# Performance work log

Hardware: AMD Instinct MI355X
Metric: run time of the kernel (lower is better)

The kernel has to match this reference:

```python
import jax, jax.numpy as jnp
import numpy as np

EMBED_DIM = 1024
NUM_HEADS = 16
HEAD_DIM = EMBED_DIM // NUM_HEADS


def setup_inputs() -> dict:
    key = jax.random.key(0)
    k1, k2, k3, k4, k5 = jax.random.split(key, 5)
    B, T, C = 4, 2048, EMBED_DIM
    scale = 1.0 / np.sqrt(C)
    return {
        "x": jax.random.normal(k1, (B, T, C), dtype=jnp.float32),
        "W_qkv": jax.random.normal(k2, (3 * C, C), dtype=jnp.float32) * scale,
        "b_qkv": jax.random.normal(k3, (3 * C,), dtype=jnp.float32) * 0.02,
        "W_proj": jax.random.normal(k4, (C, C), dtype=jnp.float32) * scale,
        "b_proj": jax.random.normal(k5, (C,), dtype=jnp.float32) * 0.02,
    }


def reference(x, W_qkv, b_qkv, W_proj, b_proj):
    B, T, C = x.shape
    H, D = NUM_HEADS, HEAD_DIM
    qkv = x @ W_qkv.T + b_qkv                      # [B,T,3C]
    q, k, v = jnp.split(qkv, 3, axis=-1)
    q = q.reshape(B, T, H, D).transpose(0, 2, 1, 3)  # [B,H,T,D]
    k = k.reshape(B, T, H, D).transpose(0, 2, 1, 3)
    v = v.reshape(B, T, H, D).transpose(0, 2, 1, 3)
    scores = jnp.einsum("bhqd,bhkd->bhqk", q, k) / np.sqrt(D)  # [B,H,T,T]
    causal = jnp.tril(jnp.ones((T, T), dtype=bool))
    scores = jnp.where(causal, scores, -jnp.inf)
    attn = jax.nn.softmax(scores, axis=-1)
    out = jnp.einsum("bhqk,bhkd->bhqd", attn, v)   # [B,H,T,D]
    out = out.transpose(0, 2, 1, 3).reshape(B, T, C)
    return out @ W_proj.T + b_proj
```

## Files before the change

kernel.cpp:

```cpp
#include <hip/hip_runtime.h>
#include <math.h>

#define EMBED 1024
#define NHEAD 16
#define HDIM  64
#define SEQT  2048
#define BATCH 4

typedef __bf16 bf16x4 __attribute__((ext_vector_type(4)));
typedef __bf16 bf16x8 __attribute__((ext_vector_type(8)));
typedef float  f32x4  __attribute__((ext_vector_type(4)));

#define AS1 __attribute__((address_space(1)))
#define AS3 __attribute__((address_space(3)))
#define GLD_LDS16(gp, lp) __builtin_amdgcn_global_load_lds( \
    (const AS1 unsigned int*)(gp), (AS3 unsigned int*)(lp), 16, 0, 0)

#define QSCALE 0.180336880f

__device__ __forceinline__ unsigned short f2bf_hw(float f) {
    union { __bf16 h; unsigned short u; } c; c.h = (__bf16)f; return c.u;
}

__global__ __launch_bounds__(256)
void cvt_all(const float* __restrict__ x, const float* __restrict__ wq,
             const float* __restrict__ wp,
             unsigned short* __restrict__ xb, unsigned short* __restrict__ wqb,
             unsigned short* __restrict__ wpb)
{
    const int N1 = 2097152;
    const int N2 = 786432;
    int i = blockIdx.x * 256 + threadIdx.x;
    const float4* src; ushort4* dst; int j;
    if (i < N1)            { src = (const float4*)x;  dst = (ushort4*)xb;  j = i; }
    else if (i < N1 + N2)  { src = (const float4*)wq; dst = (ushort4*)wqb; j = i - N1; }
    else                   { src = (const float4*)wp; dst = (ushort4*)wpb; j = i - N1 - N2; }
    float4 v = src[j];
    ushort4 o;
    o.x = f2bf_hw(v.x); o.y = f2bf_hw(v.y); o.z = f2bf_hw(v.z); o.w = f2bf_hw(v.w);
    dst[j] = o;
}

template<int MODE>
__global__ __launch_bounds__(256)
void gemm_bt_mfma(const unsigned short* __restrict__ A, const unsigned short* __restrict__ Bw,
                  const float* __restrict__ bias,
                  void* out0, void* out1, void* out2,
                  int M, int N, int K)
{
    __shared__ __align__(16) unsigned short Asm[2][128 * 32];
    __shared__ __align__(16) unsigned short Bsm[2][128 * 32];

    const int tid  = threadIdx.x;
    const int lane = tid & 63;
    const int wave = tid >> 6;
    const int wm = wave >> 1, wn = wave & 1;
    const int col = lane & 15, quad = lane >> 4;
    const long m0 = (long)blockIdx.y * 128, n0 = (long)blockIdx.x * 128;

    f32x4 acc[4][4];
#pragma unroll
    for (int mi = 0; mi < 4; mi++)
#pragma unroll
        for (int ni = 0; ni < 4; ni++) acc[mi][ni] = (f32x4){0.f, 0.f, 0.f, 0.f};

    const int lrow = tid >> 2;
    const int lcol = ((tid & 3) ^ ((tid >> 3) & 3)) * 8;
    const unsigned short* Ag = A + (m0 + lrow) * K + lcol;
    const unsigned short* Bg = Bw + (n0 + lrow) * K + lcol;

    const int rsw = (quad ^ ((col >> 1) & 3)) * 8;

    GLD_LDS16(Ag,                &Asm[0][0] + tid * 8);
    GLD_LDS16(Ag + (long)64 * K, &Asm[0][0] + 2048 + tid * 8);
    GLD_LDS16(Bg,                &Bsm[0][0] + tid * 8);
    GLD_LDS16(Bg + (long)64 * K, &Bsm[0][0] + 2048 + tid * 8);

    const int iters = K >> 5;
    for (int it = 0; it < iters; it++) {
        const int cur = it & 1;
        __builtin_amdgcn_s_waitcnt(0x0F70);
        __syncthreads();
        if (it + 1 < iters) {
            const int kk = (it + 1) * 32, nxt = cur ^ 1;
            GLD_LDS16(Ag + kk,                &Asm[nxt][0] + tid * 8);
            GLD_LDS16(Ag + (long)64 * K + kk, &Asm[nxt][0] + 2048 + tid * 8);
            GLD_LDS16(Bg + kk,                &Bsm[nxt][0] + tid * 8);
            GLD_LDS16(Bg + (long)64 * K + kk, &Bsm[nxt][0] + 2048 + tid * 8);
        }

        bf16x8 af[4], bf[4];
#pragma unroll
        for (int mi = 0; mi < 4; mi++)
            af[mi] = *(const bf16x8*)&Asm[cur][(wm * 64 + mi * 16 + col) * 32 + rsw];
#pragma unroll
        for (int ni = 0; ni < 4; ni++)
            bf[ni] = *(const bf16x8*)&Bsm[cur][(wn * 64 + ni * 16 + col) * 32 + rsw];
#pragma unroll
        for (int mi = 0; mi < 4; mi++)
#pragma unroll
            for (int ni = 0; ni < 4; ni++)
                acc[mi][ni] = __builtin_amdgcn_mfma_f32_16x16x32_bf16(af[mi], bf[ni], acc[mi][ni], 0, 0, 0);
    }

#pragma unroll
    for (int mi = 0; mi < 4; mi++) {
#pragma unroll
        for (int ni = 0; ni < 4; ni++) {
            long n = n0 + wn * 64 + ni * 16 + col;
            float bv = bias[n];
#pragma unroll
            for (int r = 0; r < 4; r++) {
                long m = m0 + wm * 64 + mi * 16 + quad * 4 + r;
                float v = acc[mi][ni][r] + bv;
                if (MODE == 0) {
                    ((float*)out0)[m * N + n] = v;
                } else {
                    int which = (int)(n >> 10);
                    int c = (int)(n & 1023);
                    int h = c >> 6, d = c & 63;
                    int b = (int)(m >> 11), t = (int)(m & 2047);
                    long bh = (long)(b * NHEAD + h);
                    if (which == 0)      ((unsigned short*)out0)[(bh * SEQT + t) * HDIM + d] = f2bf_hw(v * QSCALE);
                    else if (which == 1) ((unsigned short*)out1)[(bh * SEQT + t) * HDIM + d] = f2bf_hw(v);
                    else                 ((unsigned short*)out2)[(bh * HDIM + d) * SEQT + t] = f2bf_hw(v);
                }
            }
        }
    }
}

#define PPAD 72

__global__ __launch_bounds__(256, 3)
void flash_attn_mfma4(const unsigned short* __restrict__ Qb,
                      const unsigned short* __restrict__ Kb,
                      const unsigned short* __restrict__ Vt,
                      unsigned short* __restrict__ Ob)
{
    __shared__ __align__(16) unsigned short P_lds[128 * PPAD];
    __shared__ __align__(16) unsigned short K_lds[2][64 * 64];
    __shared__ __align__(16) unsigned short V_lds[2][64 * 64];
    __shared__ __align__(16) float L_lds[128];

    const int tid  = threadIdx.x;
    const int lane = tid & 63;
    const int wave = tid >> 6;
    const int col  = lane & 15;
    const int quad = lane >> 4;

    const int idx = blockIdx.x;
    const int qt = 15 - (idx >> 6);
    const int hb = idx & 63;
    const int h = hb & 15, b = hb >> 4;
    const int q0 = qt * 128;
    const long bh = (long)(b * NHEAD + h);
    const unsigned short* Kbh = Kb + bh * SEQT * HDIM;
    const unsigned short* Vbh = Vt + bh * HDIM * SEQT;
    const int ktiles = 2 * qt + 2;

    const int r0 = tid >> 3,         c0 = (tid & 7) ^ (r0 & 7);
    const int r1 = (tid + 256) >> 3, c1 = (tid & 7) ^ (r1 & 7);

    bf16x8 qf[2][2];
#pragma unroll
    for (int ni = 0; ni < 2; ni++) {
        const unsigned short* qrow = Qb + (bh * SEQT + q0 + wave * 32 + ni * 16 + col) * HDIM;
        qf[ni][0] = *(const bf16x8*)(qrow + quad * 8);
        qf[ni][1] = *(const bf16x8*)(qrow + 32 + quad * 8);
    }

    GLD_LDS16(Kbh + r0 * HDIM + c0 * 8,        &K_lds[0][0] + tid * 8);
    GLD_LDS16(Kbh + r1 * HDIM + c1 * 8,        &K_lds[0][0] + 2048 + tid * 8);
    GLD_LDS16(Vbh + (long)r0 * SEQT + c0 * 8,  &V_lds[0][0] + tid * 8);
    GLD_LDS16(Vbh + (long)r1 * SEQT + c1 * 8,  &V_lds[0][0] + 2048 + tid * 8);

    f32x4 o[2][4];
#pragma unroll
    for (int mi = 0; mi < 2; mi++)
#pragma unroll
        for (int dt = 0; dt < 4; dt++) o[mi][dt] = (f32x4){0.f, 0.f, 0.f, 0.f};
    float rs[2] = {0.f, 0.f};

    const int cswz0 = quad ^ (col & 7);
    const int cswz1 = (quad + 4) ^ (col & 7);

    for (int kt = 0; kt < ktiles; kt++) {
        const int cur = kt & 1;
        __builtin_amdgcn_s_waitcnt(0x0F70);
        __syncthreads();
        if (kt + 1 < ktiles) {
            const int k0n = (kt + 1) * 64, nxt = cur ^ 1;
            GLD_LDS16(Kbh + (k0n + r0) * HDIM + c0 * 8,       &K_lds[nxt][0] + tid * 8);
            GLD_LDS16(Kbh + (k0n + r1) * HDIM + c1 * 8,       &K_lds[nxt][0] + 2048 + tid * 8);
            GLD_LDS16(Vbh + (long)r0 * SEQT + k0n + c0 * 8,   &V_lds[nxt][0] + tid * 8);
            GLD_LDS16(Vbh + (long)r1 * SEQT + k0n + c1 * 8,   &V_lds[nxt][0] + 2048 + tid * 8);
        }

        const unsigned short* Kc = &K_lds[cur][0];
        f32x4 st[4][2];
        __builtin_amdgcn_s_setprio(1);
#pragma unroll
        for (int mt = 0; mt < 4; mt++) {
            const int row = mt * 16 + col;
            bf16x8 kf0 = *(const bf16x8*)&Kc[row * 64 + cswz0 * 8];
            bf16x8 kf1 = *(const bf16x8*)&Kc[row * 64 + cswz1 * 8];
#pragma unroll
            for (int ni = 0; ni < 2; ni++) {
                f32x4 acc = (f32x4){0.f, 0.f, 0.f, 0.f};
                acc = __builtin_amdgcn_mfma_f32_16x16x32_bf16(kf0, qf[ni][0], acc, 0, 0, 0);
                acc = __builtin_amdgcn_mfma_f32_16x16x32_bf16(kf1, qf[ni][1], acc, 0, 0, 0);
                st[mt][ni] = acc;
            }
        }
        __builtin_amdgcn_s_setprio(0);
        const int k0 = kt * 64;
        if (kt >= 2 * qt) {
#pragma unroll
            for (int mt = 0; mt < 4; mt++) {
                const int keybase = k0 + mt * 16 + quad * 4;
#pragma unroll
                for (int ni = 0; ni < 2; ni++) {
                    const int qg = q0 + wave * 32 + ni * 16 + col;
#pragma unroll
                    for (int r = 0; r < 4; r++)
                        if (keybase + r > qg) st[mt][ni][r] = -INFINITY;
                }
            }
        }

#pragma unroll
        for (int mt = 0; mt < 4; mt++)
#pragma unroll
            for (int ni = 0; ni < 2; ni++) {
                f32x4 p;
#pragma unroll
                for (int r = 0; r < 4; r++) p[r] = __builtin_amdgcn_exp2f(st[mt][ni][r]);
                rs[ni] += (p[0] + p[1]) + (p[2] + p[3]);
                bf16x4 pb = __builtin_convertvector(p, bf16x4);
                *(bf16x4*)&P_lds[(wave * 32 + ni * 16 + col) * PPAD + mt * 16 + quad * 4] = pb;
            }

        const unsigned short* Vc = &V_lds[cur][0];
        __builtin_amdgcn_s_setprio(1);
#pragma unroll
        for (int mi = 0; mi < 2; mi++) {
            const unsigned short* prow = &P_lds[(wave * 32 + mi * 16 + col) * PPAD];
            bf16x8 pf0 = *(const bf16x8*)(prow + quad * 8);
            bf16x8 pf1 = *(const bf16x8*)(prow + 32 + quad * 8);
#pragma unroll
            for (int dt = 0; dt < 4; dt++) {
                const int row = dt * 16 + col;
                bf16x8 vf0 = *(const bf16x8*)&Vc[row * 64 + cswz0 * 8];
                bf16x8 vf1 = *(const bf16x8*)&Vc[row * 64 + cswz1 * 8];
                o[mi][dt] = __builtin_amdgcn_mfma_f32_16x16x32_bf16(pf0, vf0, o[mi][dt], 0, 0, 0);
                o[mi][dt] = __builtin_amdgcn_mfma_f32_16x16x32_bf16(pf1, vf1, o[mi][dt], 0, 0, 0);
            }
        }
        __builtin_amdgcn_s_setprio(0);
    }

#pragma unroll
    for (int ni = 0; ni < 2; ni++) {
        rs[ni] += __shfl_xor(rs[ni], 16);
        rs[ni] += __shfl_xor(rs[ni], 32);
        if (quad == 0) L_lds[wave * 32 + ni * 16 + col] = rs[ni];
    }
    __syncthreads();
    f32x4 lf[2];
#pragma unroll
    for (int mi = 0; mi < 2; mi++)
        lf[mi] = *(const f32x4*)&L_lds[wave * 32 + mi * 16 + quad * 4];

#pragma unroll
    for (int mi = 0; mi < 2; mi++)
#pragma unroll
        for (int r = 0; r < 4; r++) {
            float inv = 1.f / lf[mi][r];
            int t = q0 + wave * 32 + mi * 16 + quad * 4 + r;
            unsigned short* orow = Ob + ((long)(b * SEQT + t)) * EMBED + h * HDIM;
#pragma unroll
            for (int dt = 0; dt < 4; dt++)
                orow[dt * 16 + col] = f2bf_hw(o[mi][dt][r] * inv);
        }
}

extern "C" void kernel_launch(void* const* d_in, const int* in_sizes, int n_in,
                              void* d_out, int out_size, void* d_ws, size_t ws_size,
                              hipStream_t stream)
{
    const float* x     = (const float*)d_in[0];
    const float* Wqkv  = (const float*)d_in[1];
    const float* bqkv  = (const float*)d_in[2];
    const float* Wproj = (const float*)d_in[3];
    const float* bproj = (const float*)d_in[4];
    float* out = (float*)d_out;

    const long Mbt = (long)BATCH * SEQT;
    const long per = (long)BATCH * NHEAD * SEQT * HDIM;

    unsigned short* xb  = (unsigned short*)d_ws;
    unsigned short* wqb = xb  + per;
    unsigned short* wpb = wqb + 3 * EMBED * EMBED;
    unsigned short* Qb  = wpb + EMBED * EMBED;
    unsigned short* Kb  = Qb + per;
    unsigned short* Vt  = Kb + per;
    unsigned short* Ob  = Vt + per;

    cvt_all<<<12288, 256, 0, stream>>>(x, Wqkv, Wproj, xb, wqb, wpb);

    dim3 g1(3 * EMBED / 128, Mbt / 128);
    gemm_bt_mfma<1><<<g1, 256, 0, stream>>>(xb, wqb, bqkv, Qb, Kb, Vt,
                                            (int)Mbt, 3 * EMBED, EMBED);

    flash_attn_mfma4<<<1024, 256, 0, stream>>>(Qb, Kb, Vt, Ob);

    dim3 g3(EMBED / 128, Mbt / 128);
    gemm_bt_mfma<0><<<g3, 256, 0, stream>>>(Ob, wpb, bproj, out, nullptr, nullptr,
                                            (int)Mbt, EMBED, EMBED);
}
```

Before: 258.1 us.

## Triple-buffer GEMM loads, skip fully masked attention tiles per wave, grid-stride convert

The projection GEMMs move from double to triple-buffered LDS staging, prefetching two k-steps ahead with one barrier per iteration and raised wave priority around the MFMA block. This is meant to hide more global-load latency. The attention kernel now lets a wave skip QK/softmax/PV work on key tiles lying entirely above its causal diagonal, while still joining the shared loads. The conversion kernel becomes a grid-stride loop with fewer blocks. Costs are more LDS per GEMM block (lower occupancy) and divergent per-wave control flow in attention.

```diff
diff --git a/kernel.cpp b/kernel.cpp
--- a/kernel.cpp
+++ b/kernel.cpp
@@ -17,6 +17,10 @@
     (const AS1 unsigned int*)(gp), (AS3 unsigned int*)(lp), 16, 0, 0)
 
 #define QSCALE 0.180336880f
+
+#define BAR do { __builtin_amdgcn_sched_barrier(0); \
+                 __builtin_amdgcn_s_barrier(); \
+                 __builtin_amdgcn_sched_barrier(0); } while (0)
 
 __device__ __forceinline__ unsigned short f2bf_hw(float f) {
     union { __bf16 h; unsigned short u; } c; c.h = (__bf16)f; return c.u;
@@ -30,26 +34,28 @@
 {
     const int N1 = 2097152;
     const int N2 = 786432;
-    int i = blockIdx.x * 256 + threadIdx.x;
-    const float4* src; ushort4* dst; int j;
-    if (i < N1)            { src = (const float4*)x;  dst = (ushort4*)xb;  j = i; }
-    else if (i < N1 + N2)  { src = (const float4*)wq; dst = (ushort4*)wqb; j = i - N1; }
-    else                   { src = (const float4*)wp; dst = (ushort4*)wpb; j = i - N1 - N2; }
-    float4 v = src[j];
-    ushort4 o;
-    o.x = f2bf_hw(v.x); o.y = f2bf_hw(v.y); o.z = f2bf_hw(v.z); o.w = f2bf_hw(v.w);
-    dst[j] = o;
+    const int NT = 3145728;
+    for (int i = blockIdx.x * 256 + threadIdx.x; i < NT; i += 2048 * 256) {
+        const float4* src; ushort4* dst; int j;
+        if (i < N1)            { src = (const float4*)x;  dst = (ushort4*)xb;  j = i; }
+        else if (i < N1 + N2)  { src = (const float4*)wq; dst = (ushort4*)wqb; j = i - N1; }
+        else                   { src = (const float4*)wp; dst = (ushort4*)wpb; j = i - N1 - N2; }
+        float4 v = src[j];
+        ushort4 o;
+        o.x = f2bf_hw(v.x); o.y = f2bf_hw(v.y); o.z = f2bf_hw(v.z); o.w = f2bf_hw(v.w);
+        dst[j] = o;
+    }
 }
 
 template<int MODE>
 __global__ __launch_bounds__(256)
-void gemm_bt_mfma(const unsigned short* __restrict__ A, const unsigned short* __restrict__ Bw,
-                  const float* __restrict__ bias,
-                  void* out0, void* out1, void* out2,
-                  int M, int N, int K)
+void gemm_bt_pipe3(const unsigned short* __restrict__ A, const unsigned short* __restrict__ Bw,
+                   const float* __restrict__ bias,
+                   void* out0, void* out1, void* out2,
+                   int M, int N, int K)
 {
-    __shared__ __align__(16) unsigned short Asm[2][128 * 32];
-    __shared__ __align__(16) unsigned short Bsm[2][128 * 32];
+    __shared__ __align__(16) unsigned short Asm[3][128 * 32];
+    __shared__ __align__(16) unsigned short Bsm[3][128 * 32];
 
     const int tid  = threadIdx.x;
     const int lane = tid & 63;
@@ -69,39 +75,51 @@
     const unsigned short* Ag = A + (m0 + lrow) * K + lcol;
     const unsigned short* Bg = Bw + (n0 + lrow) * K + lcol;
 
+#define STAGE(buf_, kk_) do { \
+    GLD_LDS16(Ag + (kk_),                &Asm[buf_][0] + tid * 8); \
+    GLD_LDS16(Ag + (long)64 * K + (kk_), &Asm[buf_][0] + 2048 + tid * 8); \
+    GLD_LDS16(Bg + (kk_),                &Bsm[buf_][0] + tid * 8); \
+    GLD_LDS16(Bg + (long)64 * K + (kk_), &Bsm[buf_][0] + 2048 + tid * 8); \
+  } while (0)
+
     const int rsw = (quad ^ ((col >> 1) & 3)) * 8;
 
-    GLD_LDS16(Ag,                &Asm[0][0] + tid * 8);
-    GLD_LDS16(Ag + (long)64 * K, &Asm[0][0] + 2048 + tid * 8);
-    GLD_LDS16(Bg,                &Bsm[0][0] + tid * 8);
-    GLD_LDS16(Bg + (long)64 * K, &Bsm[0][0] + 2048 + tid * 8);
+    STAGE(0, 0);
+    STAGE(1, 32);
+    __builtin_amdgcn_s_waitcnt(0x0F74);
+    BAR;
 
     const int iters = K >> 5;
+    int cur = 0, stg = 2;
     for (int it = 0; it < iters; it++) {
-        const int cur = it & 1;
-        __builtin_amdgcn_s_waitcnt(0x0F70);
-        __syncthreads();
-        if (it + 1 < iters) {
-            const int kk = (it + 1) * 32, nxt = cur ^ 1;
-            GLD_LDS16(Ag + kk,                &Asm[nxt][0] + tid * 8);
-            GLD_LDS16(Ag + (long)64 * K + kk, &Asm[nxt][0] + 2048 + tid * 8);
-            GLD_LDS16(Bg + kk,                &Bsm[nxt][0] + tid * 8);
-            GLD_LDS16(Bg + (long)64 * K + kk, &Bsm[nxt][0] + 2048 + tid * 8);
-        }
-
+        if (it + 2 < iters)
+            STAGE(stg, (it + 2) * 32);
+
+        const unsigned short* Ac = &Asm[cur][0];
+        const unsigned short* Bc = &Bsm[cur][0];
         bf16x8 af[4], bf[4];
 #pragma unroll
         for (int mi = 0; mi < 4; mi++)
-            af[mi] = *(const bf16x8*)&Asm[cur][(wm * 64 + mi * 16 + col) * 32 + rsw];
+            af[mi] = *(const bf16x8*)&Ac[(wm * 64 + mi * 16 + col) * 32 + rsw];
 #pragma unroll
         for (int ni = 0; ni < 4; ni++)
-            bf[ni] = *(const bf16x8*)&Bsm[cur][(wn * 64 + ni * 16 + col) * 32 + rsw];
+            bf[ni] = *(const bf16x8*)&Bc[(wn * 64 + ni * 16 + col) * 32 + rsw];
+        __builtin_amdgcn_s_setprio(1);
 #pragma unroll
         for (int mi = 0; mi < 4; mi++)
 #pragma unroll
             for (int ni = 0; ni < 4; ni++)
                 acc[mi][ni] = __builtin_amdgcn_mfma_f32_16x16x32_bf16(af[mi], bf[ni], acc[mi][ni], 0, 0, 0);
-    }
+        __builtin_amdgcn_s_setprio(0);
+
+        if (it + 2 < iters)      __builtin_amdgcn_s_waitcnt(0x0F74);
+        else if (it + 1 < iters) __builtin_amdgcn_s_waitcnt(0x0F70);
+        BAR;
+
+        cur = (cur == 2) ? 0 : cur + 1;
+        stg = (stg == 2) ? 0 : stg + 1;
+    }
+#undef STAGE
 
 #pragma unroll
     for (int mi = 0; mi < 4; mi++) {
@@ -187,6 +205,7 @@
 
     for (int kt = 0; kt < ktiles; kt++) {
         const int cur = kt & 1;
+        const int k0 = kt * 64;
         __builtin_amdgcn_s_waitcnt(0x0F70);
         __syncthreads();
         if (kt + 1 < ktiles) {
@@ -197,6 +216,8 @@
             GLD_LDS16(Vbh + (long)r1 * SEQT + k0n + c1 * 8,   &V_lds[nxt][0] + 2048 + tid * 8);
         }
 
+        if (k0 > q0 + wave * 32 + 31) continue;
+
         const unsigned short* Kc = &K_lds[cur][0];
         f32x4 st[4][2];
         __builtin_amdgcn_s_setprio(1);
@@ -214,7 +235,6 @@
             }
         }
         __builtin_amdgcn_s_setprio(0);
-        const int k0 = kt * 64;
         if (kt >= 2 * qt) {
 #pragma unroll
             for (int mt = 0; mt < 4; mt++) {
@@ -307,15 +327,15 @@
     unsigned short* Vt  = Kb + per;
     unsigned short* Ob  = Vt + per;
 
-    cvt_all<<<12288, 256, 0, stream>>>(x, Wqkv, Wproj, xb, wqb, wpb);
+    cvt_all<<<2048, 256, 0, stream>>>(x, Wqkv, Wproj, xb, wqb, wpb);
 
     dim3 g1(3 * EMBED / 128, Mbt / 128);
-    gemm_bt_mfma<1><<<g1, 256, 0, stream>>>(xb, wqb, bqkv, Qb, Kb, Vt,
-                                            (int)Mbt, 3 * EMBED, EMBED);
+    gemm_bt_pipe3<1><<<g1, 256, 0, stream>>>(xb, wqb, bqkv, Qb, Kb, Vt,
+                                             (int)Mbt, 3 * EMBED, EMBED);
 
     flash_attn_mfma4<<<1024, 256, 0, stream>>>(Qb, Kb, Vt, Ob);
 
     dim3 g3(EMBED / 128, Mbt / 128);
-    gemm_bt_mfma<0><<<g3, 256, 0, stream>>>(Ob, wpb, bproj, out, nullptr, nullptr,
-                                            (int)Mbt, EMBED, EMBED);
-}
+    gemm_bt_pipe3<0><<<g3, 256, 0, stream>>>(Ob, wpb, bproj, out, nullptr, nullptr,
+                                             (int)Mbt, EMBED, EMBED);
+}
```

After: 258.2 us. Within noise of the previous version (+0.0%).
